# Performance work log

Hardware: AMD Instinct MI355X
Metric: run time of the kernel (lower is better)

The kernel has to match this reference:

```python
import jax, jax.numpy as jnp
import numpy as np

N = 100000   # nodes
E = 800000   # edges
L = 128      # latent_size
S = 15       # message passing steps
TW = 5       # time_window
OUT = 3      # output_size
NT = 3       # node types
NODE_F = 6   # 1+1+1+NT
EDGE_F = 7   # 2+1+2+1+1


def setup_inputs() -> dict:
    key = jax.random.key(0)
    ks = iter(jax.random.split(key, 80))
    def rn(shape, s=1.0):
        return jax.random.normal(next(ks), shape, jnp.float32) * s
    w = 0.05
    d = {}
    d["pvf"] = rn((N, 1))
    d["mat_param_D"] = rn((N, 1))
    d["mat_param_X"] = rn((N, 1))
    d["node_type"] = jax.random.randint(next(ks), (N,), 0, NT)
    d["mesh_pos"] = jax.random.uniform(next(ks), (N, 2), jnp.float32)
    d["world_pos"] = jax.random.uniform(next(ks), (N, 2), jnp.float32)
    d["senders"] = jax.random.randint(next(ks), (E,), 0, N)
    d["receivers"] = jax.random.randint(next(ks), (E,), 0, N)
    # normalizer stats
    d["node_norm_mean"] = rn((NODE_F,), 0.1); d["node_norm_std"] = jnp.ones((NODE_F,), jnp.float32)
    d["edge_norm_mean"] = rn((EDGE_F,), 0.1); d["edge_norm_std"] = jnp.ones((EDGE_F,), jnp.float32)
    # node encoder
    d["ne_w1"] = rn((NODE_F, L), w); d["ne_b1"] = jnp.zeros((L,), jnp.float32)
    d["ne_w2"] = rn((L, L), w);      d["ne_b2"] = jnp.zeros((L,), jnp.float32)
    d["ne_g"] = jnp.ones((L,), jnp.float32); d["ne_be"] = jnp.zeros((L,), jnp.float32)
    # edge encoder
    d["ee_w1"] = rn((EDGE_F, L), w); d["ee_b1"] = jnp.zeros((L,), jnp.float32)
    d["ee_w2"] = rn((L, L), w);      d["ee_b2"] = jnp.zeros((L,), jnp.float32)
    d["ee_g"] = jnp.ones((L,), jnp.float32); d["ee_be"] = jnp.zeros((L,), jnp.float32)
    # stacked GraphNetBlock params (S blocks)
    d["blk_ew1"] = rn((S, 3 * L, L), w); d["blk_eb1"] = jnp.zeros((S, L), jnp.float32)
    d["blk_ew2"] = rn((S, L, L), w);     d["blk_eb2"] = jnp.zeros((S, L), jnp.float32)
    d["blk_eg"] = jnp.ones((S, L), jnp.float32); d["blk_ebt"] = jnp.zeros((S, L), jnp.float32)
    d["blk_nw1"] = rn((S, 2 * L, L), w); d["blk_nb1"] = jnp.zeros((S, L), jnp.float32)
    d["blk_nw2"] = rn((S, L, L), w);     d["blk_nb2"] = jnp.zeros((S, L), jnp.float32)
    d["blk_ng"] = jnp.ones((S, L), jnp.float32); d["blk_nbt"] = jnp.zeros((S, L), jnp.float32)
    # decoder (Conv1d k=1 == per-node Linear)
    d["dec_w1"] = rn((L, 8), w); d["dec_b1"] = jnp.zeros((8,), jnp.float32)
    d["dec_w2"] = rn((8, OUT * TW), w); d["dec_b2"] = jnp.zeros((OUT * TW,), jnp.float32)
    return d


def _mlp_ln(x, w1, b1, w2, b2, g, b):
    # Linear-ReLU-Linear-ReLU-LayerNorm
    h = jax.nn.relu(x @ w1 + b1)
    h = jax.nn.relu(h @ w2 + b2)
    mu = jnp.mean(h, axis=-1, keepdims=True)
    var = jnp.var(h, axis=-1, keepdims=True)
    return (h - mu) * jax.lax.rsqrt(var + 1e-5) * g + b


def _forward(pvf, mat_param_D, mat_param_X, node_type, mesh_pos, world_pos, senders, receivers,
             node_norm_mean, node_norm_std, edge_norm_mean, edge_norm_std,
             ne_w1, ne_b1, ne_w2, ne_b2, ne_g, ne_be,
             ee_w1, ee_b1, ee_w2, ee_b2, ee_g, ee_be,
             blk_ew1, blk_eb1, blk_ew2, blk_eb2, blk_eg, blk_ebt,
             blk_nw1, blk_nb1, blk_nw2, blk_nb2, blk_ng, blk_nbt,
             dec_w1, dec_b1, dec_w2, dec_b2):
    # --- build features ---
    one_hot = jax.nn.one_hot(node_type, NT, dtype=jnp.float32)
    node_feats = jnp.concatenate([pvf, mat_param_D, mat_param_X, one_hot], axis=-1)   # [N, NODE_F]
    rel_m = mesh_pos[senders] - mesh_pos[receivers]
    dist_m = jnp.linalg.norm(rel_m, axis=-1, keepdims=True)
    rel_w = world_pos[senders] - world_pos[receivers]
    dist_w = jnp.linalg.norm(rel_w, axis=-1, keepdims=True)
    pvf_grad = pvf[senders] - pvf[receivers]
    edge_feats = jnp.concatenate([rel_m, dist_m, rel_w, dist_w, pvf_grad], axis=-1)   # [E, EDGE_F]
    # --- encode ---
    nl = _mlp_ln((node_feats - node_norm_mean) / node_norm_std, ne_w1, ne_b1, ne_w2, ne_b2, ne_g, ne_be)
    el = _mlp_ln((edge_feats - edge_norm_mean) / edge_norm_std, ee_w1, ee_b1, ee_w2, ee_b2, ee_g, ee_be)
    # --- process: S GraphNetBlocks with residuals ---
    def step(carry, p):
        nl, el = carry
        ew1, eb1, ew2, eb2, eg, ebt, nw1, nb1, nw2, nb2, ng, nbt = p
        edge_in = jnp.concatenate([nl[senders], nl[receivers], el], axis=-1)          # [E, 3L]
        new_e = _mlp_ln(edge_in, ew1, eb1, ew2, eb2, eg, ebt)
        aggr = jax.ops.segment_sum(new_e, receivers, num_segments=N)                  # [N, L]
        new_n = _mlp_ln(jnp.concatenate([nl, aggr], axis=-1), nw1, nb1, nw2, nb2, ng, nbt)
        return (nl + new_n, el + new_e), None
    (nl, el), _ = jax.lax.scan(step, (nl, el),
                               (blk_ew1, blk_eb1, blk_ew2, blk_eb2, blk_eg, blk_ebt,
                                blk_nw1, blk_nb1, blk_nw2, blk_nb2, blk_ng, blk_nbt))
    # --- decode (Conv1d k=1 == Linear) ---
    h = nl @ dec_w1 + dec_b1
    h = h * jax.nn.sigmoid(h)                                                         # Swish beta=1
    decoded = h @ dec_w2 + dec_b2                                                     # [N, OUT*TW]
    dt = jnp.repeat(jnp.arange(1, TW + 1, dtype=jnp.float32), OUT)                    # repeat_interleave
    delta = (decoded * dt).reshape(N, TW, OUT).transpose(1, 0, 2)                     # [TW, N, OUT]
    return delta


def reference(pvf, mat_param_D, mat_param_X, node_type, mesh_pos, world_pos, senders, receivers,
              node_norm_mean, node_norm_std, edge_norm_mean, edge_norm_std,
              ne_w1, ne_b1, ne_w2, ne_b2, ne_g, ne_be,
              ee_w1, ee_b1, ee_w2, ee_b2, ee_g, ee_be,
              blk_ew1, blk_eb1, blk_ew2, blk_eb2, blk_eg, blk_ebt,
              blk_nw1, blk_nb1, blk_nw2, blk_nb2, blk_ng, blk_nbt,
              dec_w1, dec_b1, dec_w2, dec_b2):
    return _forward(pvf, mat_param_D, mat_param_X, node_type, mesh_pos, world_pos, senders, receivers,
                    node_norm_mean, node_norm_std, edge_norm_mean, edge_norm_std,
                    ne_w1, ne_b1, ne_w2, ne_b2, ne_g, ne_be,
                    ee_w1, ee_b1, ee_w2, ee_b2, ee_g, ee_be,
                    blk_ew1, blk_eb1, blk_ew2, blk_eb2, blk_eg, blk_ebt,
                    blk_nw1, blk_nb1, blk_nw2, blk_nb2, blk_ng, blk_nbt,
                    dec_w1, dec_b1, dec_w2, dec_b2)
```

## Files before the change

### kernel.cpp

```cpp
#include <hip/hip_runtime.h>
#include <math.h>

#define NNODES 100000
#define NEDGES 800000
#define L 128
#define NBSCAN ((NNODES + 255) / 256)

typedef unsigned short u16;
typedef unsigned int u32;
typedef unsigned short ushort8 __attribute__((ext_vector_type(8)));
typedef _Float16 f16x8 __attribute__((ext_vector_type(8)));
typedef __attribute__((ext_vector_type(4))) float f32x4;

static __device__ __forceinline__ float h2f(u16 u) {
    _Float16 h;
    __builtin_memcpy(&h, &u, 2);
    return (float)h;
}
static __device__ __forceinline__ u16 f2h(float x) {
    _Float16 h = (_Float16)x;
    u16 u;
    __builtin_memcpy(&u, &h, 2);
    return u;
}
static __device__ __forceinline__ void load8h(const u16* p, float* d) {
    ushort8 v = *(const ushort8*)p;
    #pragma unroll
    for (int k = 0; k < 8; k++) d[k] = h2f(v[k]);
}
static __device__ __forceinline__ void atomic_pk_add_f16(u16* addr, u32 data) {
    asm volatile("global_atomic_pk_add_f16 %0, %1, off" :: "v"(addr), "v"(data));
}

__global__ __launch_bounds__(256) void zero_kernel(uint4* p, int n) {
    int i = blockIdx.x * 256 + threadIdx.x;
    if (i < n) p[i] = make_uint4(0u, 0u, 0u, 0u);
}

__global__ __launch_bounds__(256) void diag_kernel(float* out, int n, float val) {
    int i = blockIdx.x * 256 + threadIdx.x;
    if (i < n) out[i] = val;
}

__global__ __launch_bounds__(256) void count_kernel(
    const int* __restrict__ receivers, u32* __restrict__ counts)
{
    int e = blockIdx.x * 256 + threadIdx.x;
    if (e < NEDGES) atomicAdd(&counts[receivers[e]], 1u);
}

__global__ __launch_bounds__(256) void scan_block_kernel(
    const u32* __restrict__ counts, u32* __restrict__ offsets,
    u32* __restrict__ partials)
{
    __shared__ u32 sh[256];
    int i = blockIdx.x * 256 + threadIdx.x;
    u32 c = (i < NNODES) ? counts[i] : 0u;
    sh[threadIdx.x] = c;
    __syncthreads();
    #pragma unroll
    for (int d = 1; d < 256; d <<= 1) {
        u32 v = (threadIdx.x >= d) ? sh[threadIdx.x - d] : 0u;
        __syncthreads();
        sh[threadIdx.x] += v;
        __syncthreads();
    }
    if (i < NNODES) offsets[i] = sh[threadIdx.x] - c;
    if (threadIdx.x == 255) partials[blockIdx.x] = sh[255];
}

__global__ __launch_bounds__(512) void scan_partials_kernel(u32* __restrict__ partials)
{
    __shared__ u32 sh[512];
    int x = threadIdx.x;
    u32 c = (x < NBSCAN) ? partials[x] : 0u;
    sh[x] = c;
    __syncthreads();
    #pragma unroll
    for (int d = 1; d < 512; d <<= 1) {
        u32 v = (x >= d) ? sh[x - d] : 0u;
        __syncthreads();
        sh[x] += v;
        __syncthreads();
    }
    if (x < NBSCAN) partials[x] = sh[x] - c;
}

__global__ __launch_bounds__(256) void add_offsets_kernel(
    u32* __restrict__ offsets, const u32* __restrict__ partials,
    u32* __restrict__ cursor)
{
    int i = blockIdx.x * 256 + threadIdx.x;
    if (i < NNODES) {
        u32 v = offsets[i] + partials[blockIdx.x];
        offsets[i] = v;
        cursor[i] = v;
    }
}

__global__ __launch_bounds__(256) void scatter_kernel(
    const int* __restrict__ senders, const int* __restrict__ receivers,
    u32* __restrict__ cursor, int* __restrict__ ssorted, int* __restrict__ rsorted)
{
    int e = blockIdx.x * 256 + threadIdx.x;
    if (e < NEDGES) {
        int r = receivers[e];
        u32 pos = atomicAdd(&cursor[r], 1u);
        ssorted[pos] = senders[e];
        rsorted[pos] = r;
    }
}

__global__ __launch_bounds__(256) void pack_weights_kernel(
    const float* __restrict__ src, u16* __restrict__ dst, int K, int nsteps)
{
    int idx = blockIdx.x * 256 + threadIdx.x;
    int nkk = K >> 5;
    int total = nsteps * 8 * nkk * 64;
    if (idx >= total) return;
    int lane = idx & 63;
    int rest = idx >> 6;
    int kk = rest % nkk; rest /= nkk;
    int nb = rest & 7;
    int s = rest >> 3;
    int c15 = lane & 15, gg = lane >> 4;
    const float* w = src + (size_t)s * K * 128;
    u16 out[8];
    #pragma unroll
    for (int j = 0; j < 8; j++) {
        int k = kk * 32 + gg * 8 + j;
        out[j] = f2h(w[(size_t)k * 128 + nb * 16 + c15]);
    }
    *(ushort8*)(dst + (size_t)idx * 8) = *(ushort8*)out;
}

__global__ __launch_bounds__(256) void node_encode_kernel(
    const float* __restrict__ pvf, const float* __restrict__ matD,
    const float* __restrict__ matX, const int* __restrict__ ntype,
    const float* __restrict__ nmean, const float* __restrict__ nstd,
    const float* __restrict__ w1, const float* __restrict__ b1,
    const float* __restrict__ w2, const float* __restrict__ b2,
    const float* __restrict__ g, const float* __restrict__ be,
    u16* __restrict__ nl)
{
    __shared__ float xs[64][8];
    __shared__ float h[64][132];
    const int t = threadIdx.x;
    const int base = blockIdx.x * 64;
    if (t < 64) {
        int n = base + t;
        if (n < NNODES) {
            int nt = ntype[n];
            float f[6];
            f[0] = pvf[n]; f[1] = matD[n]; f[2] = matX[n];
            f[3] = (nt == 0) ? 1.f : 0.f;
            f[4] = (nt == 1) ? 1.f : 0.f;
            f[5] = (nt == 2) ? 1.f : 0.f;
            #pragma unroll
            for (int k = 0; k < 6; k++) xs[t][k] = (f[k] - nmean[k]) / nstd[k];
        } else {
            #pragma unroll
            for (int k = 0; k < 6; k++) xs[t][k] = 0.f;
        }
    }
    __syncthreads();
    const int j = t & 127, half = t >> 7;
    for (int i = 0; i < 32; i++) {
        int e = half * 32 + i;
        float acc = b1[j];
        #pragma unroll
        for (int k = 0; k < 6; k++) acc += xs[e][k] * w1[k * L + j];
        h[e][j] = fmaxf(acc, 0.f);
    }
    __syncthreads();
    float acc2[32];
    #pragma unroll
    for (int i = 0; i < 32; i++) acc2[i] = b2[j];
    for (int k4 = 0; k4 < 32; k4++) {
        const float* wp = w2 + k4 * 4 * L + j;
        float wa = wp[0], wb = wp[L], wc = wp[2 * L], wd = wp[3 * L];
        #pragma unroll
        for (int i = 0; i < 32; i++) {
            const float4 xv = *(const float4*)&h[half * 32 + i][k4 * 4];
            acc2[i] += xv.x * wa + xv.y * wb + xv.z * wc + xv.w * wd;
        }
    }
    __syncthreads();
    #pragma unroll
    for (int i = 0; i < 32; i++) h[half * 32 + i][j] = fmaxf(acc2[i], 0.f);
    __syncthreads();
    {
        const int e = t >> 2, tg = t & 3;
        float sum = 0.f, sq = 0.f;
        #pragma unroll
        for (int jj = 0; jj < 32; jj++) { float v = h[e][tg * 32 + jj]; sum += v; sq += v * v; }
        sum += __shfl_xor(sum, 1); sq += __shfl_xor(sq, 1);
        sum += __shfl_xor(sum, 2); sq += __shfl_xor(sq, 2);
        float mu = sum * (1.f / 128.f);
        float rstd = rsqrtf(sq * (1.f / 128.f) - mu * mu + 1e-5f);
        int n = base + e;
        if (n < NNODES) {
            u32* nrow = (u32*)(nl + (size_t)n * L) + tg * 16;
            #pragma unroll
            for (int p = 0; p < 16; p++) {
                int f0 = tg * 32 + 2 * p;
                float v0 = (h[e][f0] - mu) * rstd * g[f0] + be[f0];
                float v1 = (h[e][f0 + 1] - mu) * rstd * g[f0 + 1] + be[f0 + 1];
                nrow[p] = (u32)f2h(v0) | ((u32)f2h(v1) << 16);
            }
        }
    }
}

__global__ __launch_bounds__(256) void edge_encode_kernel(
    const int* __restrict__ ssorted, const int* __restrict__ rsorted,
    const float* __restrict__ pvf, const float* __restrict__ mesh,
    const float* __restrict__ world,
    const float* __restrict__ emean, const float* __restrict__ estd,
    const float* __restrict__ w1, const float* __restrict__ b1,
    const float* __restrict__ w2, const float* __restrict__ b2,
    const float* __restrict__ g, const float* __restrict__ be,
    u16* __restrict__ el)
{
    __shared__ float xs[64][8];
    __shared__ float h[64][132];
    const int t = threadIdx.x;
    const int base = blockIdx.x * 64;
    if (t < 64) {
        int e = base + t;
        int s = ssorted[e], r = rsorted[e];
        float rmx = mesh[s * 2] - mesh[r * 2];
        float rmy = mesh[s * 2 + 1] - mesh[r * 2 + 1];
        float dm = sqrtf(rmx * rmx + rmy * rmy);
        float rwx = world[s * 2] - world[r * 2];
        float rwy = world[s * 2 + 1] - world[r * 2 + 1];
        float dw = sqrtf(rwx * rwx + rwy * rwy);
        float pg = pvf[s] - pvf[r];
        float f[7] = {rmx, rmy, dm, rwx, rwy, dw, pg};
        #pragma unroll
        for (int k = 0; k < 7; k++) xs[t][k] = (f[k] - emean[k]) / estd[k];
    }
    __syncthreads();
    const int j = t & 127, half = t >> 7;
    for (int i = 0; i < 32; i++) {
        int e = half * 32 + i;
        float acc = b1[j];
        #pragma unroll
        for (int k = 0; k < 7; k++) acc += xs[e][k] * w1[k * L + j];
        h[e][j] = fmaxf(acc, 0.f);
    }
    __syncthreads();
    float acc2[32];
    #pragma unroll
    for (int i = 0; i < 32; i++) acc2[i] = b2[j];
    for (int k4 = 0; k4 < 32; k4++) {
        const float* wp = w2 + k4 * 4 * L + j;
        float wa = wp[0], wb = wp[L], wc = wp[2 * L], wd = wp[3 * L];
        #pragma unroll
        for (int i = 0; i < 32; i++) {
            const float4 xv = *(const float4*)&h[half * 32 + i][k4 * 4];
            acc2[i] += xv.x * wa + xv.y * wb + xv.z * wc + xv.w * wd;
        }
    }
    __syncthreads();
    #pragma unroll
    for (int i = 0; i < 32; i++) h[half * 32 + i][j] = fmaxf(acc2[i], 0.f);
    __syncthreads();
    {
        const int e = t >> 2, tg = t & 3;
        float sum = 0.f, sq = 0.f;
        #pragma unroll
        for (int jj = 0; jj < 32; jj++) { float v = h[e][tg * 32 + jj]; sum += v; sq += v * v; }
        sum += __shfl_xor(sum, 1); sq += __shfl_xor(sq, 1);
        sum += __shfl_xor(sum, 2); sq += __shfl_xor(sq, 2);
        float mu = sum * (1.f / 128.f);
        float rstd = rsqrtf(sq * (1.f / 128.f) - mu * mu + 1e-5f);
        u32* erow = (u32*)(el + (size_t)(base + e) * L) + tg * 16;
        #pragma unroll
        for (int p = 0; p < 16; p++) {
            int f0 = tg * 32 + 2 * p;
            float v0 = (h[e][f0] - mu) * rstd * g[f0] + be[f0];
            float v1 = (h[e][f0 + 1] - mu) * rstd * g[f0 + 1] + be[f0 + 1];
            erow[p] = (u32)f2h(v0) | ((u32)f2h(v1) << 16);
        }
    }
}

#define EDGE_LOAD_A(nk, slot)                                                     \
    {                                                                             \
        _Pragma("unroll")                                                         \
        for (int m = 0; m < 4; m++) {                                             \
            const u16* ap;                                                        \
            if ((nk) < 4)      ap = nl + (size_t)sA[m] * L + (nk) * 32 + g * 8;   \
            else if ((nk) < 8) ap = nl + (size_t)rA[m] * L + ((nk) - 4) * 32 + g * 8; \
            else               ap = el + (size_t)(base + m * 16 + c15) * L + ((nk) - 8) * 32 + g * 8; \
            ab[slot][m] = *(const f16x8*)ap;                                      \
        }                                                                         \
    }

#define NODE_LOAD_A(nk, slot)                                                     \
    {                                                                             \
        _Pragma("unroll")                                                         \
        for (int m = 0; m < 4; m++) {                                             \
            const u16* ap = ((nk) < 4) ? (nl + (size_t)rowL[m] * L + (nk) * 32 + g * 8) \
                                       : (aggr + (size_t)rowL[m] * L + ((nk) - 4) * 32 + g * 8); \
            ab[slot][m] = *(const f16x8*)ap;                                      \
        }                                                                         \
    }

#define LGKM_BARRIER()                                          \
    asm volatile("s_waitcnt lgkmcnt(0)" ::: "memory");          \
    __builtin_amdgcn_sched_barrier(0);                          \
    __builtin_amdgcn_s_barrier();

__global__ __launch_bounds__(256, 2) void edge_block_kernel(
    const int* __restrict__ ssorted, const int* __restrict__ rsorted,
    const u16* __restrict__ nl, u16* __restrict__ el, u16* __restrict__ aggr,
    const u16* __restrict__ wp1, const float* __restrict__ b1,
    const u16* __restrict__ wp2, const float* __restrict__ b2,
    const float* __restrict__ gamma, const float* __restrict__ beta)
{
    __shared__ __align__(16) u16 wbuf[2][8][64][8];
    __shared__ __align__(16) u16 hbuf[4][2][4][64][8];
    const int t = threadIdx.x;
    const int wid = t >> 6, lane = t & 63;
    const int c15 = lane & 15, g = lane >> 4;
    const int base = blockIdx.x * 256 + wid * 64;

    int sA[4], rA[4];
    #pragma unroll
    for (int m = 0; m < 4; m++) {
        sA[m] = ssorted[base + m * 16 + c15];
        rA[m] = rsorted[base + m * 16 + c15];
    }

    f32x4 acc[8][4];
    #pragma unroll
    for (int nb = 0; nb < 8; nb++) {
        float bv = b1[nb * 16 + c15];
        #pragma unroll
        for (int m = 0; m < 4; m++) acc[nb][m] = (f32x4){bv, bv, bv, bv};
    }
    f16x8 ab[2][4];
    f16x8 w0, w1;
    w0 = *(const f16x8*)(wp1 + ((size_t)((2 * wid) * 12 + 0) * 64 + lane) * 8);
    w1 = *(const f16x8*)(wp1 + ((size_t)((2 * wid + 1) * 12 + 0) * 64 + lane) * 8);
    EDGE_LOAD_A(0, 0);
    *(f16x8*)&wbuf[0][2 * wid][lane][0] = w0;
    *(f16x8*)&wbuf[0][2 * wid + 1][lane][0] = w1;
    LGKM_BARRIER();

    #pragma unroll
    for (int kk = 0; kk < 12; kk++) {
        if (kk < 11) {
            w0 = *(const f16x8*)(wp1 + ((size_t)((2 * wid) * 12 + kk + 1) * 64 + lane) * 8);
            w1 = *(const f16x8*)(wp1 + ((size_t)((2 * wid + 1) * 12 + kk + 1) * 64 + lane) * 8);
            EDGE_LOAD_A(kk + 1, (kk + 1) & 1);
        }
        __builtin_amdgcn_s_setprio(1);
        #pragma unroll
        for (int nb = 0; nb < 8; nb++) {
            f16x8 b = *(const f16x8*)&wbuf[kk & 1][nb][lane][0];
            #pragma unroll
            for (int m = 0; m < 4; m++)
                acc[nb][m] = __builtin_amdgcn_mfma_f32_16x16x32_f16(ab[kk & 1][m], b, acc[nb][m], 0, 0, 0);
        }
        __builtin_amdgcn_s_setprio(0);
        if (kk < 11) {
            *(f16x8*)&wbuf[(kk + 1) & 1][2 * wid][lane][0] = w0;
            *(f16x8*)&wbuf[(kk + 1) & 1][2 * wid + 1][lane][0] = w1;
            LGKM_BARRIER();
        }
    }

    float gamv[8], btv[8];
    #pragma unroll
    for (int nb = 0; nb < 8; nb++) {
        gamv[nb] = gamma[nb * 16 + c15];
        btv[nb] = beta[nb * 16 + c15];
    }
    #pragma unroll
    for (int mp = 0; mp < 2; mp++) {
        #pragma unroll
        for (int ml = 0; ml < 2; ml++) {
            int m = mp * 2 + ml;
            #pragma unroll
            for (int nb = 0; nb < 8; nb++) {
                int kk2 = nb >> 1;
                int sub = ((nb & 1) << 1) | (c15 >> 3);
                int jj = c15 & 7;
                #pragma unroll
                for (int i = 0; i < 4; i++) {
                    float v = fmaxf(acc[nb][m][i], 0.f);
                    hbuf[wid][ml][kk2][g * 4 + i + 16 * sub][jj] = f2h(v);
                }
            }
        }
        f32x4 acc2[2][8];
        #pragma unroll
        for (int nb = 0; nb < 8; nb++) {
            float bv = b2[nb * 16 + c15];
            acc2[0][nb] = (f32x4){bv, bv, bv, bv};
            acc2[1][nb] = (f32x4){bv, bv, bv, bv};
        }
        __builtin_amdgcn_s_setprio(1);
        #pragma unroll
        for (int kk = 0; kk < 4; kk++) {
            f16x8 a0 = *(const f16x8*)&hbuf[wid][0][kk][lane][0];
            f16x8 a1 = *(const f16x8*)&hbuf[wid][1][kk][lane][0];
            #pragma unroll
            for (int nb = 0; nb < 8; nb++) {
                f16x8 b = *(const f16x8*)(wp2 + ((size_t)(nb * 4 + kk) * 64 + lane) * 8);
                acc2[0][nb] = __builtin_amdgcn_mfma_f32_16x16x32_f16(a0, b, acc2[0][nb], 0, 0, 0);
                acc2[1][nb] = __builtin_amdgcn_mfma_f32_16x16x32_f16(a1, b, acc2[1][nb], 0, 0, 0);
            }
        }
        __builtin_amdgcn_s_setprio(0);
        #pragma unroll
        for (int ml = 0; ml < 2; ml++) {
            const int slot = mp * 2 + ml;
            float muv[4], rsv[4];
            #pragma unroll
            for (int i = 0; i < 4; i++) {
                float p = 0.f, q = 0.f;
                #pragma unroll
                for (int nb = 0; nb < 8; nb++) {
                    float v = fmaxf(acc2[ml][nb][i], 0.f);
                    acc2[ml][nb][i] = v;
                    p += v; q += v * v;
                }
                p += __shfl_xor(p, 1); q += __shfl_xor(q, 1);
                p += __shfl_xor(p, 2); q += __shfl_xor(q, 2);
                p += __shfl_xor(p, 4); q += __shfl_xor(q, 4);
                p += __shfl_xor(p, 8); q += __shfl_xor(q, 8);
                float mu = p * (1.f / 128.f);
                muv[i] = mu;
                rsv[i] = rsqrtf(q * (1.f / 128.f) - mu * mu + 1e-5f);
            }
            float av[8], apv[8];
            #pragma unroll
            for (int nb = 0; nb < 8; nb++) { av[nb] = 0.f; apv[nb] = 0.f; }
            int cur = rsorted[base + slot * 16 + g * 4];
            #pragma unroll
            for (int i = 0; i < 4; i++) {
                int erow = base + slot * 16 + g * 4 + i;
                int ri = (i == 0) ? cur : rsorted[erow];
                float vv[8], pp[8];
                #pragma unroll
                for (int nb = 0; nb < 8; nb++) {
                    float v = (acc2[ml][nb][i] - muv[i]) * rsv[i] * gamv[nb] + btv[nb];
                    vv[nb] = v;
                    pp[nb] = __shfl_xor(v, 1);
                }
                u32 olds[8];
                if (!(c15 & 1)) {
                    #pragma unroll
                    for (int nb = 0; nb < 8; nb++)
                        olds[nb] = *(const u32*)(el + (size_t)erow * L + nb * 16 + c15);
                }
                if (ri != cur) {
                    #pragma unroll
                    for (int nb = 0; nb < 8; nb++) {
                        if (!(c15 & 1)) {
                            u32 add = (u32)f2h(av[nb]) | ((u32)f2h(apv[nb]) << 16);
                            atomic_pk_add_f16(aggr + (size_t)cur * L + nb * 16 + c15, add);
                        }
                        av[nb] = 0.f; apv[nb] = 0.f;
                    }
                    cur = ri;
                }
                #pragma unroll
                for (int nb = 0; nb < 8; nb++) {
                    av[nb] += vv[nb];
                    apv[nb] += pp[nb];
                    if (!(c15 & 1)) {
                        float r0 = h2f((u16)(olds[nb] & 0xFFFFu)) + vv[nb];
                        float r1 = h2f((u16)(olds[nb] >> 16)) + pp[nb];
                        *(u32*)(el + (size_t)erow * L + nb * 16 + c15) =
                            (u32)f2h(r0) | ((u32)f2h(r1) << 16);
                    }
                }
            }
            #pragma unroll
            for (int nb = 0; nb < 8; nb++) {
                if (!(c15 & 1)) {
                    u32 add = (u32)f2h(av[nb]) | ((u32)f2h(apv[nb]) << 16);
                    atomic_pk_add_f16(aggr + (size_t)cur * L + nb * 16 + c15, add);
                }
            }
        }
    }
}

__global__ __launch_bounds__(256, 2) void node_block_kernel(
    u16* __restrict__ nl, u16* __restrict__ aggr,
    const u16* __restrict__ wp1, const float* __restrict__ b1,
    const u16* __restrict__ wp2, const float* __restrict__ b2,
    const float* __restrict__ gamma, const float* __restrict__ beta)
{
    __shared__ __align__(16) u16 wbuf[2][8][64][8];
    __shared__ __align__(16) u16 hbuf[4][2][4][64][8];
    const int t = threadIdx.x;
    const int wid = t >> 6, lane = t & 63;
    const int c15 = lane & 15, g = lane >> 4;
    const int base = blockIdx.x * 256 + wid * 64;

    int rowL[4];
    #pragma unroll
    for (int m = 0; m < 4; m++) {
        int r = base + m * 16 + c15;
        rowL[m] = r < NNODES ? r : 0;
    }

    f32x4 acc[8][4];
    #pragma unroll
    for (int nb = 0; nb < 8; nb++) {
        float bv = b1[nb * 16 + c15];
        #pragma unroll
        for (int m = 0; m < 4; m++) acc[nb][m] = (f32x4){bv, bv, bv, bv};
    }
    f16x8 ab[2][4];
    f16x8 w0, w1;
    w0 = *(const f16x8*)(wp1 + ((size_t)((2 * wid) * 8 + 0) * 64 + lane) * 8);
    w1 = *(const f16x8*)(wp1 + ((size_t)((2 * wid + 1) * 8 + 0) * 64 + lane) * 8);
    NODE_LOAD_A(0, 0);
    *(f16x8*)&wbuf[0][2 * wid][lane][0] = w0;
    *(f16x8*)&wbuf[0][2 * wid + 1][lane][0] = w1;
    LGKM_BARRIER();

    #pragma unroll
    for (int kk = 0; kk < 8; kk++) {
        if (kk < 7) {
            w0 = *(const f16x8*)(wp1 + ((size_t)((2 * wid) * 8 + kk + 1) * 64 + lane) * 8);
            w1 = *(const f16x8*)(wp1 + ((size_t)((2 * wid + 1) * 8 + kk + 1) * 64 + lane) * 8);
            NODE_LOAD_A(kk + 1, (kk + 1) & 1);
        }
        __builtin_amdgcn_s_setprio(1);
        #pragma unroll
        for (int nb = 0; nb < 8; nb++) {
            f16x8 b = *(const f16x8*)&wbuf[kk & 1][nb][lane][0];
            #pragma unroll
            for (int m = 0; m < 4; m++)
                acc[nb][m] = __builtin_amdgcn_mfma_f32_16x16x32_f16(ab[kk & 1][m], b, acc[nb][m], 0, 0, 0);
        }
        __builtin_amdgcn_s_setprio(0);
        if (kk < 7) {
            *(f16x8*)&wbuf[(kk + 1) & 1][2 * wid][lane][0] = w0;
            *(f16x8*)&wbuf[(kk + 1) & 1][2 * wid + 1][lane][0] = w1;
            LGKM_BARRIER();
        }
    }

    {
        const uint4 z4 = make_uint4(0u, 0u, 0u, 0u);
        #pragma unroll
        for (int m = 0; m < 4; m++) {
            int r = base + m * 16 + c15;
            if (r < NNODES) {
                #pragma unroll
                for (int kk = 0; kk < 4; kk++)
                    *(uint4*)(aggr + (size_t)r * L + kk * 32 + g * 8) = z4;
            }
        }
    }

    float gamv[8], btv[8];
    #pragma unroll
    for (int nb = 0; nb < 8; nb++) {
        gamv[nb] = gamma[nb * 16 + c15];
        btv[nb] = beta[nb * 16 + c15];
    }
    #pragma unroll
    for (int mp = 0; mp < 2; mp++) {
        #pragma unroll
        for (int ml = 0; ml < 2; ml++) {
            int m = mp * 2 + ml;
            #pragma unroll
            for (int nb = 0; nb < 8; nb++) {
                int kk2 = nb >> 1;
                int sub = ((nb & 1) << 1) | (c15 >> 3);
                int jj = c15 & 7;
                #pragma unroll
                for (int i = 0; i < 4; i++) {
                    float v = fmaxf(acc[nb][m][i], 0.f);
                    hbuf[wid][ml][kk2][g * 4 + i + 16 * sub][jj] = f2h(v);
                }
            }
        }
        f32x4 acc2[2][8];
        #pragma unroll
        for (int nb = 0; nb < 8; nb++) {
            float bv = b2[nb * 16 + c15];
            acc2[0][nb] = (f32x4){bv, bv, bv, bv};
            acc2[1][nb] = (f32x4){bv, bv, bv, bv};
        }
        __builtin_amdgcn_s_setprio(1);
        #pragma unroll
        for (int kk = 0; kk < 4; kk++) {
            f16x8 a0 = *(const f16x8*)&hbuf[wid][0][kk][lane][0];
            f16x8 a1 = *(const f16x8*)&hbuf[wid][1][kk][lane][0];
            #pragma unroll
            for (int nb = 0; nb < 8; nb++) {
                f16x8 b = *(const f16x8*)(wp2 + ((size_t)(nb * 4 + kk) * 64 + lane) * 8);
                acc2[0][nb] = __builtin_amdgcn_mfma_f32_16x16x32_f16(a0, b, acc2[0][nb], 0, 0, 0);
                acc2[1][nb] = __builtin_amdgcn_mfma_f32_16x16x32_f16(a1, b, acc2[1][nb], 0, 0, 0);
            }
        }
        __builtin_amdgcn_s_setprio(0);
        #pragma unroll
        for (int ml = 0; ml < 2; ml++) {
            float muv[4], rsv[4];
            #pragma unroll
            for (int i = 0; i < 4; i++) {
                float p = 0.f, q = 0.f;
                #pragma unroll
                for (int nb = 0; nb < 8; nb++) {
                    float v = fmaxf(acc2[ml][nb][i], 0.f);
                    acc2[ml][nb][i] = v;
                    p += v; q += v * v;
                }
                p += __shfl_xor(p, 1); q += __shfl_xor(q, 1);
                p += __shfl_xor(p, 2); q += __shfl_xor(q, 2);
                p += __shfl_xor(p, 4); q += __shfl_xor(q, 4);
                p += __shfl_xor(p, 8); q += __shfl_xor(q, 8);
                float mu = p * (1.f / 128.f);
                muv[i] = mu;
                rsv[i] = rsqrtf(q * (1.f / 128.f) - mu * mu + 1e-5f);
            }
            #pragma unroll
            for (int i = 0; i < 4; i++) {
                int nrow = base + (mp * 2 + ml) * 16 + g * 4 + i;
                #pragma unroll
                for (int nb = 0; nb < 8; nb++) {
                    float v = (acc2[ml][nb][i] - muv[i]) * rsv[i] * gamv[nb] + btv[nb];
                    float pv = __shfl_xor(v, 1);
                    if (!(c15 & 1) && nrow < NNODES) {
                        int col = nb * 16 + c15;
                        u32* nlp = (u32*)(nl + (size_t)nrow * L + col);
                        u32 old = *nlp;
                        float r0 = h2f((u16)(old & 0xFFFFu)) + v;
                        float r1 = h2f((u16)(old >> 16)) + pv;
                        *nlp = (u32)f2h(r0) | ((u32)f2h(r1) << 16);
                    }
                }
            }
        }
    }
}

__global__ __launch_bounds__(256) void decode_kernel(
    const u16* __restrict__ nl,
    const float* __restrict__ w1, const float* __restrict__ b1,
    const float* __restrict__ w2, const float* __restrict__ b2,
    float* __restrict__ out)
{
    int n = blockIdx.x * blockDim.x + threadIdx.x;
    if (n >= NNODES) return;
    float h8[8];
    #pragma unroll
    for (int jj = 0; jj < 8; jj++) h8[jj] = b1[jj];
    const u16* row = nl + (size_t)n * L;
    for (int k = 0; k < L; k += 8) {
        float xv[8];
        load8h(row + k, xv);
        #pragma unroll
        for (int q = 0; q < 8; q++)
            #pragma unroll
            for (int jj = 0; jj < 8; jj++)
                h8[jj] += xv[q] * w1[(k + q) * 8 + jj];
    }
    #pragma unroll
    for (int jj = 0; jj < 8; jj++) { float v = h8[jj]; h8[jj] = v / (1.f + expf(-v)); }
    #pragma unroll
    for (int o15 = 0; o15 < 15; o15++) {
        float accv = b2[o15];
        #pragma unroll
        for (int jj = 0; jj < 8; jj++) accv += h8[jj] * w2[jj * 15 + o15];
        int tt = o15 / 3, oo = o15 - tt * 3;
        out[(size_t)tt * NNODES * 3 + (size_t)n * 3 + oo] = accv * (float)(tt + 1);
    }
}

extern "C" void kernel_launch(void* const* d_in, const int* in_sizes, int n_in,
                              void* d_out, int out_size, void* d_ws, size_t ws_size,
                              hipStream_t stream)
{
    const size_t AG_B = (size_t)NNODES * L * 2;
    const size_t EL_B = (size_t)NEDGES * L * 2;
    const size_t NL_B = (size_t)NNODES * L * 2;
    const size_t PE1_N = (size_t)15 * 8 * 12 * 64 * 8;
    const size_t PE2_N = (size_t)15 * 8 * 4 * 64 * 8;
    const size_t PN1_N = (size_t)15 * 8 * 8 * 64 * 8;
    const size_t PN2_N = (size_t)15 * 8 * 4 * 64 * 8;
    const size_t WPK_B = (PE1_N + PE2_N + PN1_N + PN2_N) * 2;
    const size_t SS_B  = (size_t)NEDGES * 4;
    const size_t RS_B  = (size_t)NEDGES * 4;
    const size_t CNT_B = (size_t)NNODES * 4;
    const size_t OFF_B = (size_t)NNODES * 4;
    const size_t CUR_B = (size_t)NNODES * 4;
    const size_t PAR_B = 2048;
    const size_t TOTAL = AG_B + EL_B + NL_B + WPK_B + SS_B + RS_B
                       + CNT_B + OFF_B + CUR_B + PAR_B;

    if (ws_size < TOTAL) {
        float val = 1000.0f + (float)((double)ws_size * 1e-6);
        diag_kernel<<<(out_size + 255) / 256, 256, 0, stream>>>((float*)d_out, out_size, val);
        return;
    }

    char* wsp = (char*)d_ws;
    u16* aggr = (u16*)wsp;                 wsp += AG_B;
    u16* el   = (u16*)wsp;                 wsp += EL_B;
    u16* nl   = (u16*)wsp;                 wsp += NL_B;
    u16* pe1  = (u16*)wsp;                 wsp += PE1_N * 2;
    u16* pe2  = (u16*)wsp;                 wsp += PE2_N * 2;
    u16* pn1  = (u16*)wsp;                 wsp += PN1_N * 2;
    u16* pn2  = (u16*)wsp;                 wsp += PN2_N * 2;
    int* ssorted = (int*)wsp;              wsp += SS_B;
    int* rsorted = (int*)wsp;              wsp += RS_B;
    u32* counts  = (u32*)wsp;              wsp += CNT_B;
    u32* offsets = (u32*)wsp;              wsp += OFF_B;
    u32* cursor  = (u32*)wsp;              wsp += CUR_B;
    u32* partials = (u32*)wsp;             wsp += PAR_B;
    float* out = (float*)d_out;

    const float* pvf       = (const float*)d_in[0];
    const float* matD      = (const float*)d_in[1];
    const float* matX      = (const float*)d_in[2];
    const int*   ntype     = (const int*)d_in[3];
    const float* mesh      = (const float*)d_in[4];
    const float* world     = (const float*)d_in[5];
    const int*   senders   = (const int*)d_in[6];
    const int*   receivers = (const int*)d_in[7];
    const float* nmean = (const float*)d_in[8];
    const float* nstd  = (const float*)d_in[9];
    const float* emean = (const float*)d_in[10];
    const float* estd  = (const float*)d_in[11];
    const float* ne_w1 = (const float*)d_in[12];
    const float* ne_b1 = (const float*)d_in[13];
    const float* ne_w2 = (const float*)d_in[14];
    const float* ne_b2 = (const float*)d_in[15];
    const float* ne_g  = (const float*)d_in[16];
    const float* ne_be = (const float*)d_in[17];
    const float* ee_w1 = (const float*)d_in[18];
    const float* ee_b1 = (const float*)d_in[19];
    const float* ee_w2 = (const float*)d_in[20];
    const float* ee_b2 = (const float*)d_in[21];
    const float* ee_g  = (const float*)d_in[22];
    const float* ee_be = (const float*)d_in[23];
    const float* blk_ew1 = (const float*)d_in[24];
    const float* blk_eb1 = (const float*)d_in[25];
    const float* blk_ew2 = (const float*)d_in[26];
    const float* blk_eb2 = (const float*)d_in[27];
    const float* blk_eg  = (const float*)d_in[28];
    const float* blk_ebt = (const float*)d_in[29];
    const float* blk_nw1 = (const float*)d_in[30];
    const float* blk_nb1 = (const float*)d_in[31];
    const float* blk_nw2 = (const float*)d_in[32];
    const float* blk_nb2 = (const float*)d_in[33];
    const float* blk_ng  = (const float*)d_in[34];
    const float* blk_nbt = (const float*)d_in[35];
    const float* dec_w1 = (const float*)d_in[36];
    const float* dec_b1 = (const float*)d_in[37];
    const float* dec_w2 = (const float*)d_in[38];
    const float* dec_b2 = (const float*)d_in[39];

    zero_kernel<<<(int)((CNT_B / 16 + 255) / 256), 256, 0, stream>>>((uint4*)counts, (int)(CNT_B / 16));
    count_kernel<<<(NEDGES + 255) / 256, 256, 0, stream>>>(receivers, counts);
    scan_block_kernel<<<NBSCAN, 256, 0, stream>>>(counts, offsets, partials);
    scan_partials_kernel<<<1, 512, 0, stream>>>(partials);
    add_offsets_kernel<<<NBSCAN, 256, 0, stream>>>(offsets, partials, cursor);
    scatter_kernel<<<(NEDGES + 255) / 256, 256, 0, stream>>>(senders, receivers, cursor, ssorted, rsorted);

    pack_weights_kernel<<<(int)((15 * 8 * 12 * 64 + 255) / 256), 256, 0, stream>>>(
        blk_ew1, pe1, 384, 15);
    pack_weights_kernel<<<(int)((15 * 8 * 4 * 64 + 255) / 256), 256, 0, stream>>>(
        blk_ew2, pe2, 128, 15);
    pack_weights_kernel<<<(int)((15 * 8 * 8 * 64 + 255) / 256), 256, 0, stream>>>(
        blk_nw1, pn1, 256, 15);
    pack_weights_kernel<<<(int)((15 * 8 * 4 * 64 + 255) / 256), 256, 0, stream>>>(
        blk_nw2, pn2, 128, 15);

    node_encode_kernel<<<(NNODES + 63) / 64, 256, 0, stream>>>(
        pvf, matD, matX, ntype, nmean, nstd,
        ne_w1, ne_b1, ne_w2, ne_b2, ne_g, ne_be, nl);
    edge_encode_kernel<<<NEDGES / 64, 256, 0, stream>>>(
        ssorted, rsorted, pvf, mesh, world, emean, estd,
        ee_w1, ee_b1, ee_w2, ee_b2, ee_g, ee_be, el);

    const int nzero = NNODES * L * 2 / 16;
    zero_kernel<<<(nzero + 255) / 256, 256, 0, stream>>>((uint4*)aggr, nzero);

    for (int s = 0; s < 15; s++) {
        edge_block_kernel<<<NEDGES / 256, 256, 0, stream>>>(
            ssorted, rsorted, nl, el, aggr,
            pe1 + (size_t)s * 8 * 12 * 64 * 8, blk_eb1 + s * L,
            pe2 + (size_t)s * 8 * 4 * 64 * 8,  blk_eb2 + s * L,
            blk_eg + s * L, blk_ebt + s * L);
        node_block_kernel<<<(NNODES + 255) / 256, 256, 0, stream>>>(
            nl, aggr,
            pn1 + (size_t)s * 8 * 8 * 64 * 8, blk_nb1 + s * L,
            pn2 + (size_t)s * 8 * 4 * 64 * 8, blk_nb2 + s * L,
            blk_ng + s * L, blk_nbt + s * L);
    }

    decode_kernel<<<(NNODES + 255) / 256, 256, 0, stream>>>(
        nl, dec_w1, dec_b1, dec_w2, dec_b2, out);
}
```

Measured before the change: 7.313 ms.

## Rewrite edge encoder MLP with fp16 MFMA and packed weights

Replaces the scalar fp32 edge-encoder MLP with an MFMA-based version. Both layers use packed fp16 weights, and the first layer's 7 inputs are zero-padded to K=32. Each wave now handles 64 edges. Hidden activations go through a small LDS buffer, and layernorm is computed with cross-lane shuffles. The goal is to cut the encoder's FP32 ALU cost, at the price of fp16 precision for the inputs and hidden activations.

New measurement: 6.844 ms (median of 2 runs). -6.4%, faster.

```diff
diff --git a/kernel.cpp b/kernel.cpp
--- a/kernel.cpp
+++ b/kernel.cpp
@@ -130,6 +130,22 @@
     for (int j = 0; j < 8; j++) {
         int k = kk * 32 + gg * 8 + j;
         out[j] = f2h(w[(size_t)k * 128 + nb * 16 + c15]);
+    }
+    *(ushort8*)(dst + (size_t)idx * 8) = *(ushort8*)out;
+}
+
+__global__ __launch_bounds__(256) void pack_ee1_kernel(
+    const float* __restrict__ src, u16* __restrict__ dst)
+{
+    int idx = blockIdx.x * 256 + threadIdx.x;
+    if (idx >= 8 * 64) return;
+    int lane = idx & 63, nb = idx >> 6;
+    int c15 = lane & 15, gg = lane >> 4;
+    u16 out[8];
+    #pragma unroll
+    for (int j = 0; j < 8; j++) {
+        int k = gg * 8 + j;
+        out[j] = (k < 7) ? f2h(src[(size_t)k * 128 + nb * 16 + c15]) : (u16)0;
     }
     *(ushort8*)(dst + (size_t)idx * 8) = *(ushort8*)out;
 }
@@ -212,76 +228,135 @@
     }
 }
 
-__global__ __launch_bounds__(256) void edge_encode_kernel(
+__global__ __launch_bounds__(256, 2) void edge_encode_kernel(
     const int* __restrict__ ssorted, const int* __restrict__ rsorted,
     const float* __restrict__ pvf, const float* __restrict__ mesh,
     const float* __restrict__ world,
     const float* __restrict__ emean, const float* __restrict__ estd,
-    const float* __restrict__ w1, const float* __restrict__ b1,
-    const float* __restrict__ w2, const float* __restrict__ b2,
-    const float* __restrict__ g, const float* __restrict__ be,
+    const u16* __restrict__ wp1, const float* __restrict__ b1,
+    const u16* __restrict__ wp2, const float* __restrict__ b2,
+    const float* __restrict__ gamma, const float* __restrict__ beta,
     u16* __restrict__ el)
 {
-    __shared__ float xs[64][8];
-    __shared__ float h[64][132];
+    __shared__ __align__(16) u16 hbuf[4][2][4][64][8];
     const int t = threadIdx.x;
-    const int base = blockIdx.x * 64;
-    if (t < 64) {
-        int e = base + t;
-        int s = ssorted[e], r = rsorted[e];
-        float rmx = mesh[s * 2] - mesh[r * 2];
-        float rmy = mesh[s * 2 + 1] - mesh[r * 2 + 1];
-        float dm = sqrtf(rmx * rmx + rmy * rmy);
-        float rwx = world[s * 2] - world[r * 2];
-        float rwy = world[s * 2 + 1] - world[r * 2 + 1];
-        float dw = sqrtf(rwx * rwx + rwy * rwy);
-        float pg = pvf[s] - pvf[r];
-        float f[7] = {rmx, rmy, dm, rwx, rwy, dw, pg};
-        #pragma unroll
-        for (int k = 0; k < 7; k++) xs[t][k] = (f[k] - emean[k]) / estd[k];
-    }
-    __syncthreads();
-    const int j = t & 127, half = t >> 7;
-    for (int i = 0; i < 32; i++) {
-        int e = half * 32 + i;
-        float acc = b1[j];
-        #pragma unroll
-        for (int k = 0; k < 7; k++) acc += xs[e][k] * w1[k * L + j];
-        h[e][j] = fmaxf(acc, 0.f);
-    }
-    __syncthreads();
-    float acc2[32];
-    #pragma unroll
-    for (int i = 0; i < 32; i++) acc2[i] = b2[j];
-    for (int k4 = 0; k4 < 32; k4++) {
-        const float* wp = w2 + k4 * 4 * L + j;
-        float wa = wp[0], wb = wp[L], wc = wp[2 * L], wd = wp[3 * L];
-        #pragma unroll
-        for (int i = 0; i < 32; i++) {
-            const float4 xv = *(const float4*)&h[half * 32 + i][k4 * 4];
-            acc2[i] += xv.x * wa + xv.y * wb + xv.z * wc + xv.w * wd;
-        }
-    }
-    __syncthreads();
-    #pragma unroll
-    for (int i = 0; i < 32; i++) h[half * 32 + i][j] = fmaxf(acc2[i], 0.f);
-    __syncthreads();
-    {
-        const int e = t >> 2, tg = t & 3;
-        float sum = 0.f, sq = 0.f;
-        #pragma unroll
-        for (int jj = 0; jj < 32; jj++) { float v = h[e][tg * 32 + jj]; sum += v; sq += v * v; }
-        sum += __shfl_xor(sum, 1); sq += __shfl_xor(sq, 1);
-        sum += __shfl_xor(sum, 2); sq += __shfl_xor(sq, 2);
-        float mu = sum * (1.f / 128.f);
-        float rstd = rsqrtf(sq * (1.f / 128.f) - mu * mu + 1e-5f);
-        u32* erow = (u32*)(el + (size_t)(base + e) * L) + tg * 16;
-        #pragma unroll
-        for (int p = 0; p < 16; p++) {
-            int f0 = tg * 32 + 2 * p;
-            float v0 = (h[e][f0] - mu) * rstd * g[f0] + be[f0];
-            float v1 = (h[e][f0 + 1] - mu) * rstd * g[f0 + 1] + be[f0 + 1];
-            erow[p] = (u32)f2h(v0) | ((u32)f2h(v1) << 16);
+    const int wid = t >> 6, lane = t & 63;
+    const int c15 = lane & 15, g = lane >> 4;
+    const int base = blockIdx.x * 256 + wid * 64;
+
+    f16x8 a[4];
+    #pragma unroll
+    for (int m = 0; m < 4; m++) {
+        f16x8 v;
+        #pragma unroll
+        for (int k = 0; k < 8; k++) v[k] = (_Float16)0.f;
+        if (g == 0) {
+            int e = base + m * 16 + c15;
+            int s = ssorted[e], r = rsorted[e];
+            float rmx = mesh[s * 2] - mesh[r * 2];
+            float rmy = mesh[s * 2 + 1] - mesh[r * 2 + 1];
+            float dm = sqrtf(rmx * rmx + rmy * rmy);
+            float rwx = world[s * 2] - world[r * 2];
+            float rwy = world[s * 2 + 1] - world[r * 2 + 1];
+            float dw = sqrtf(rwx * rwx + rwy * rwy);
+            float pg = pvf[s] - pvf[r];
+            float f[7] = {rmx, rmy, dm, rwx, rwy, dw, pg};
+            #pragma unroll
+            for (int k = 0; k < 7; k++)
+                v[k] = (_Float16)((f[k] - emean[k]) / estd[k]);
+        }
+        a[m] = v;
+    }
+
+    f32x4 acc[8][4];
+    #pragma unroll
+    for (int nb = 0; nb < 8; nb++) {
+        float bv = b1[nb * 16 + c15];
+        #pragma unroll
+        for (int m = 0; m < 4; m++) acc[nb][m] = (f32x4){bv, bv, bv, bv};
+    }
+    #pragma unroll
+    for (int nb = 0; nb < 8; nb++) {
+        f16x8 b = *(const f16x8*)(wp1 + ((size_t)(nb * 64 + lane)) * 8);
+        #pragma unroll
+        for (int m = 0; m < 4; m++)
+            acc[nb][m] = __builtin_amdgcn_mfma_f32_16x16x32_f16(a[m], b, acc[nb][m], 0, 0, 0);
+    }
+
+    float gamv[8], btv[8];
+    #pragma unroll
+    for (int nb = 0; nb < 8; nb++) {
+        gamv[nb] = gamma[nb * 16 + c15];
+        btv[nb] = beta[nb * 16 + c15];
+    }
+    #pragma unroll
+    for (int mp = 0; mp < 2; mp++) {
+        #pragma unroll
+        for (int ml = 0; ml < 2; ml++) {
+            int m = mp * 2 + ml;
+            #pragma unroll
+            for (int nb = 0; nb < 8; nb++) {
+                int kk2 = nb >> 1;
+                int sub = ((nb & 1) << 1) | (c15 >> 3);
+                int jj = c15 & 7;
+                #pragma unroll
+                for (int i = 0; i < 4; i++) {
+                    float v = fmaxf(acc[nb][m][i], 0.f);
+                    hbuf[wid][ml][kk2][g * 4 + i + 16 * sub][jj] = f2h(v);
+                }
+            }
+        }
+        f32x4 acc2[2][8];
+        #pragma unroll
+        for (int nb = 0; nb < 8; nb++) {
+            float bv = b2[nb * 16 + c15];
+            acc2[0][nb] = (f32x4){bv, bv, bv, bv};
+            acc2[1][nb] = (f32x4){bv, bv, bv, bv};
+        }
+        #pragma unroll
+        for (int kk = 0; kk < 4; kk++) {
+            f16x8 a0 = *(const f16x8*)&hbuf[wid][0][kk][lane][0];
+            f16x8 a1 = *(const f16x8*)&hbuf[wid][1][kk][lane][0];
+            #pragma unroll
+            for (int nb = 0; nb < 8; nb++) {
+                f16x8 b = *(const f16x8*)(wp2 + ((size_t)(nb * 4 + kk) * 64 + lane) * 8);
+                acc2[0][nb] = __builtin_amdgcn_mfma_f32_16x16x32_f16(a0, b, acc2[0][nb], 0, 0, 0);
+                acc2[1][nb] = __builtin_amdgcn_mfma_f32_16x16x32_f16(a1, b, acc2[1][nb], 0, 0, 0);
+            }
+        }
+        #pragma unroll
+        for (int ml = 0; ml < 2; ml++) {
+            float muv[4], rsv[4];
+            #pragma unroll
+            for (int i = 0; i < 4; i++) {
+                float p = 0.f, q = 0.f;
+                #pragma unroll
+                for (int nb = 0; nb < 8; nb++) {
+                    float v = fmaxf(acc2[ml][nb][i], 0.f);
+                    acc2[ml][nb][i] = v;
+                    p += v; q += v * v;
+                }
+                p += __shfl_xor(p, 1); q += __shfl_xor(q, 1);
+                p += __shfl_xor(p, 2); q += __shfl_xor(q, 2);
+                p += __shfl_xor(p, 4); q += __shfl_xor(q, 4);
+                p += __shfl_xor(p, 8); q += __shfl_xor(q, 8);
+                float mu = p * (1.f / 128.f);
+                muv[i] = mu;
+                rsv[i] = rsqrtf(q * (1.f / 128.f) - mu * mu + 1e-5f);
+            }
+            #pragma unroll
+            for (int i = 0; i < 4; i++) {
+                int erow = base + (mp * 2 + ml) * 16 + g * 4 + i;
+                #pragma unroll
+                for (int nb = 0; nb < 8; nb++) {
+                    float v = (acc2[ml][nb][i] - muv[i]) * rsv[i] * gamv[nb] + btv[nb];
+                    float pv = __shfl_xor(v, 1);
+                    if (!(c15 & 1)) {
+                        *(u32*)(el + (size_t)erow * L + nb * 16 + c15) =
+                            (u32)f2h(v) | ((u32)f2h(pv) << 16);
+                    }
+                }
+            }
         }
     }
 }
@@ -692,7 +767,9 @@
     const size_t PE2_N = (size_t)15 * 8 * 4 * 64 * 8;
     const size_t PN1_N = (size_t)15 * 8 * 8 * 64 * 8;
     const size_t PN2_N = (size_t)15 * 8 * 4 * 64 * 8;
-    const size_t WPK_B = (PE1_N + PE2_N + PN1_N + PN2_N) * 2;
+    const size_t PEE1_N = (size_t)8 * 64 * 8;
+    const size_t PEE2_N = (size_t)8 * 4 * 64 * 8;
+    const size_t WPK_B = (PE1_N + PE2_N + PN1_N + PN2_N + PEE1_N + PEE2_N) * 2;
     const size_t SS_B  = (size_t)NEDGES * 4;
     const size_t RS_B  = (size_t)NEDGES * 4;
     const size_t CNT_B = (size_t)NNODES * 4;
@@ -716,6 +793,8 @@
     u16* pe2  = (u16*)wsp;                 wsp += PE2_N * 2;
     u16* pn1  = (u16*)wsp;                 wsp += PN1_N * 2;
     u16* pn2  = (u16*)wsp;                 wsp += PN2_N * 2;
+    u16* pee1 = (u16*)wsp;                 wsp += PEE1_N * 2;
+    u16* pee2 = (u16*)wsp;                 wsp += PEE2_N * 2;
     int* ssorted = (int*)wsp;              wsp += SS_B;
     int* rsorted = (int*)wsp;              wsp += RS_B;
     u32* counts  = (u32*)wsp;              wsp += CNT_B;
@@ -780,13 +859,16 @@
         blk_nw1, pn1, 256, 15);
     pack_weights_kernel<<<(int)((15 * 8 * 4 * 64 + 255) / 256), 256, 0, stream>>>(
         blk_nw2, pn2, 128, 15);
+    pack_ee1_kernel<<<2, 256, 0, stream>>>(ee_w1, pee1);
+    pack_weights_kernel<<<(int)((8 * 4 * 64 + 255) / 256), 256, 0, stream>>>(
+        ee_w2, pee2, 128, 1);
 
     node_encode_kernel<<<(NNODES + 63) / 64, 256, 0, stream>>>(
         pvf, matD, matX, ntype, nmean, nstd,
         ne_w1, ne_b1, ne_w2, ne_b2, ne_g, ne_be, nl);
-    edge_encode_kernel<<<NEDGES / 64, 256, 0, stream>>>(
+    edge_encode_kernel<<<NEDGES / 256, 256, 0, stream>>>(
         ssorted, rsorted, pvf, mesh, world, emean, estd,
-        ee_w1, ee_b1, ee_w2, ee_b2, ee_g, ee_be, el);
+        pee1, ee_b1, pee2, ee_b2, ee_g, ee_be, el);
 
     const int nzero = NNODES * L * 2 / 16;
     zero_kernel<<<(nzero + 255) / 256, 256, 0, stream>>>((uint4*)aggr, nzero);
```
